# Optimization experiments

Measured on AMD Instinct MI355X. Metric: run time of the kernel, lower is better.

Reference implementation:

```python
import jax, jax.numpy as jnp
import numpy as np

D = 1024
H = 16
HD = D // H  # 64
FF = 4 * D
EPS = 1e-5


def _xavier(key, shape):
    fan_in, fan_out = shape[1], shape[0]
    limit = float(np.sqrt(6.0 / (fan_in + fan_out)))
    return jax.random.uniform(key, shape, jnp.float32, -limit, limit)


def setup_inputs() -> dict:
    key = jax.random.key(0)
    ks = jax.random.split(key, 8)
    x = jax.random.normal(ks[0], (2, 2048, D), jnp.float32)
    return {
        "x": x,
        "w_qkv": _xavier(ks[1], (3 * D, D)),
        "b_qkv": jnp.zeros((3 * D,), jnp.float32),
        "w_out": _xavier(ks[2], (D, D)),
        "b_out": jnp.zeros((D,), jnp.float32),
        "w1": _xavier(ks[3], (FF, D)),
        "b1": jnp.zeros((FF,), jnp.float32),
        "w2": _xavier(ks[4], (D, FF)),
        "b2": jnp.zeros((D,), jnp.float32),
        "ln1_g": jnp.ones((D,), jnp.float32),
        "ln1_b": jnp.zeros((D,), jnp.float32),
        "ln2_g": jnp.ones((D,), jnp.float32),
        "ln2_b": jnp.zeros((D,), jnp.float32),
    }


def _layernorm(x, g, b):
    mu = jnp.mean(x, -1, keepdims=True)
    var = jnp.mean(jnp.square(x - mu), -1, keepdims=True)
    return (x - mu) * jax.lax.rsqrt(var + EPS) * g + b


def reference(x, w_qkv, b_qkv, w_out, b_out, w1, b1, w2, b2,
              ln1_g, ln1_b, ln2_g, ln2_b):
    B, S, _ = x.shape
    # pre-LN attention branch
    h = _layernorm(x, ln1_g, ln1_b)
    qkv = h @ w_qkv.T + b_qkv                      # [B,S,3D]
    qkv = qkv.reshape(B, S, H, 3 * HD).transpose(0, 2, 1, 3)  # [B,H,S,3hd]
    q, k, v = jnp.split(qkv, 3, axis=-1)
    scores = jnp.einsum('bhqd,bhkd->bhqk', q, k) / np.sqrt(HD)
    attn = jax.nn.softmax(scores, axis=-1)
    ctx = jnp.einsum('bhqk,bhkd->bhqd', attn, v)   # [B,H,S,hd]
    ctx = ctx.transpose(0, 2, 1, 3).reshape(B, S, D)
    x = x + (ctx @ w_out.T + b_out)
    # pre-LN MLP branch
    h = _layernorm(x, ln2_g, ln2_b)
    h = jax.nn.relu(h @ w1.T + b1)
    x = x + (h @ w2.T + b2)
    return x
```

## Files before the change

### kernel.cpp

```cpp
#include <hip/hip_runtime.h>
#include <hip/hip_bf16.h>

typedef __attribute__((ext_vector_type(8))) short bf16x8;
typedef __attribute__((ext_vector_type(4))) float f32x4;
typedef __attribute__((ext_vector_type(16))) float f32x16;
typedef __attribute__((ext_vector_type(4))) unsigned short u16x4;
typedef __attribute__((ext_vector_type(4))) unsigned int u32x4;
typedef unsigned short u16;

__device__ __forceinline__ u16 f2bf(float f) {
  unsigned u = __builtin_bit_cast(unsigned, f);
  u += 0x7fffu + ((u >> 16) & 1u);
  return (u16)(u >> 16);
}
__device__ __forceinline__ float bf2f(u16 u) {
  unsigned v = ((unsigned)u) << 16;
  return __builtin_bit_cast(float, v);
}
__device__ __forceinline__ unsigned cvt_pk_bf16(float lo, float hi) {
  unsigned r;
  asm("v_cvt_pk_bf16_f32 %0, %1, %2" : "=v"(r) : "v"(lo), "v"(hi));
  return r;
}
__device__ __forceinline__ float exp2_fast(float x) {
  float r;
  asm("v_exp_f32 %0, %1" : "=v"(r) : "v"(x));
  return r;
}

__device__ __forceinline__ void gl_lds16(const void* g, void* l) {
  __builtin_amdgcn_global_load_lds((const __attribute__((address_space(1))) void*)g,
                                   (__attribute__((address_space(3))) void*)l,
                                   16, 0, 0);
}

__device__ __forceinline__ void bar() {
  asm volatile("" ::: "memory");
  __builtin_amdgcn_s_barrier();
  asm volatile("" ::: "memory");
}

__global__ __launch_bounds__(256) void ln_cvt(const float* __restrict__ x,
                                              const float* __restrict__ g,
                                              const float* __restrict__ b,
                                              u16* __restrict__ out,
                                              const float* __restrict__ wa,
                                              const float* __restrict__ wb,
                                              const float* __restrict__ wc,
                                              const float* __restrict__ wd,
                                              u16* __restrict__ oa,
                                              u16* __restrict__ ob,
                                              u16* __restrict__ oc,
                                              u16* __restrict__ od) {
  __shared__ float red[8];
  const int t = threadIdx.x;
  if (blockIdx.x < 4096) {
    const int row = blockIdx.x;
    const int lane = t & 63, w = t >> 6;
    const float4 v = ((const float4*)(x + (size_t)row * 1024))[t];
    float s = v.x + v.y + v.z + v.w;
    float q = v.x * v.x + v.y * v.y + v.z * v.z + v.w * v.w;
#pragma unroll
    for (int off = 32; off; off >>= 1) {
      s += __shfl_down(s, off);
      q += __shfl_down(q, off);
    }
    if (lane == 0) { red[w] = s; red[4 + w] = q; }
    __syncthreads();
    s = red[0] + red[1] + red[2] + red[3];
    q = red[4] + red[5] + red[6] + red[7];
    const float mu = s * (1.f / 1024.f);
    const float var = q * (1.f / 1024.f) - mu * mu;
    const float rs = rsqrtf(var + 1e-5f);
    const float4 gv = ((const float4*)g)[t];
    const float4 bv = ((const float4*)b)[t];
    u16x4 o;
    o.x = f2bf((v.x - mu) * rs * gv.x + bv.x);
    o.y = f2bf((v.y - mu) * rs * gv.y + bv.y);
    o.z = f2bf((v.z - mu) * rs * gv.z + bv.z);
    o.w = f2bf((v.w - mu) * rs * gv.w + bv.w);
    ((u16x4*)(out + (size_t)row * 1024))[t] = o;
  } else {
    int i = (blockIdx.x - 4096) * 256 + t;
    const int stride = 2048 * 256;
    for (; i < 3145728; i += stride) {
      const float* src;
      u16* dst;
      int j;
      if (i < 786432) { src = wa; dst = oa; j = i; }
      else if (i < 1048576) { src = wb; dst = ob; j = i - 786432; }
      else if (i < 2097152) { src = wc; dst = oc; j = i - 1048576; }
      else { src = wd; dst = od; j = i - 2097152; }
      float4 v = ((const float4*)src)[j];
      u16x4 o;
      o.x = f2bf(v.x); o.y = f2bf(v.y); o.z = f2bf(v.z); o.w = f2bf(v.w);
      ((u16x4*)dst)[j] = o;
    }
  }
}

__global__ __launch_bounds__(256) void ln_k(const float* __restrict__ x,
                                            const float* __restrict__ g,
                                            const float* __restrict__ b,
                                            u16* __restrict__ out) {
  const int row = blockIdx.x;
  const int t = threadIdx.x;
  const int lane = t & 63, w = t >> 6;
  const float4 v = ((const float4*)(x + (size_t)row * 1024))[t];
  float s = v.x + v.y + v.z + v.w;
  float q = v.x * v.x + v.y * v.y + v.z * v.z + v.w * v.w;
#pragma unroll
  for (int off = 32; off; off >>= 1) {
    s += __shfl_down(s, off);
    q += __shfl_down(q, off);
  }
  __shared__ float red[8];
  if (lane == 0) { red[w] = s; red[4 + w] = q; }
  __syncthreads();
  s = red[0] + red[1] + red[2] + red[3];
  q = red[4] + red[5] + red[6] + red[7];
  const float mu = s * (1.f / 1024.f);
  const float var = q * (1.f / 1024.f) - mu * mu;
  const float rs = rsqrtf(var + 1e-5f);
  const float4 gv = ((const float4*)g)[t];
  const float4 bv = ((const float4*)b)[t];
  u16x4 o;
  o.x = f2bf((v.x - mu) * rs * gv.x + bv.x);
  o.y = f2bf((v.y - mu) * rs * gv.y + bv.y);
  o.z = f2bf((v.z - mu) * rs * gv.z + bv.z);
  o.w = f2bf((v.w - mu) * rs * gv.w + bv.w);
  ((u16x4*)(out + (size_t)row * 1024))[t] = o;
}

template <int EPI>
__global__ __launch_bounds__(512, 2) void gemm8(const u16* __restrict__ A,
                                                const u16* __restrict__ B,
                                                const float* __restrict__ bias,
                                                void* __restrict__ outp,
                                                const int N, const int K) {
  __shared__ u16 lds[65536];
  const int t = threadIdx.x;
  const int lane = t & 63, w = t >> 6;
  const int wm = w >> 2, wn = w & 3;
  const int l15 = lane & 15, lhi = lane >> 4;
  const int nbx = gridDim.x;
  const int nwg = nbx * gridDim.y;
  const int orig = blockIdx.y * nbx + blockIdx.x;
  const int cpx = nwg >> 3;
  const int lid = (orig & 7) * cpx + (orig >> 3);
  const long bm = (long)(lid / nbx) * 256, bn = (long)(lid % nbx) * 256;
  const u16* Ab = A + bm * K;
  const u16* Bb = B + bn * K;
  const int nt = K >> 6;
  const int ni2 = nt >> 1;

  const int srow0 = t >> 3, sg0 = (t & 7) ^ (srow0 & 7);
  const int srow1 = 64 + srow0, sg1 = (t & 7) ^ (srow1 & 7);

#define STAGE8(Mb, hf, kt_, dstb)                                             \
  do {                                                                        \
    const long kk_ = (long)(kt_) << 6;                                        \
    gl_lds16(Mb + (size_t)((hf) * 128 + srow0) * K + kk_ + sg0 * 8,           \
             &lds[(dstb) + w * 512]);                                         \
    gl_lds16(Mb + (size_t)((hf) * 128 + srow1) * K + kk_ + sg1 * 8,           \
             &lds[(dstb) + 4096 + w * 512]);                                  \
  } while (0)

#define LOADA(db, mi, fk0, fk1)                                               \
  {                                                                           \
    const int r_ = (mi) * 16 + l15;                                           \
    const int b_ = ((db) * 2 + wm) * 8192 + r_ * 64;                          \
    fk0 = *(const bf16x8*)&lds[b_ + ((lhi ^ (r_ & 7)) << 3)];                 \
    fk1 = *(const bf16x8*)&lds[b_ + (((4 + lhi) ^ (r_ & 7)) << 3)];           \
  }

#define LOADB(db)                                                             \
  _Pragma("unroll")                                                           \
  for (int ni = 0; ni < 4; ++ni) {                                            \
    const int R_ = wn * 64 + ni * 16 + l15;                                   \
    const int b_ = 32768 + ((db) * 2 + (R_ >> 7)) * 8192 + (R_ & 127) * 64;   \
    bq[ni][0] = *(const bf16x8*)&lds[b_ + ((lhi ^ (R_ & 7)) << 3)];           \
    bq[ni][1] = *(const bf16x8*)&lds[b_ + (((4 + lhi) ^ (R_ & 7)) << 3)];     \
  }

#define MM(q, a0k0, a0k1, a1k0, a1k1)                                         \
  __builtin_amdgcn_s_setprio(1);                                              \
  _Pragma("unroll")                                                           \
  for (int ni = 0; ni < 4; ++ni) {                                            \
    acc[2 * (q)][ni] = __builtin_amdgcn_mfma_f32_16x16x32_bf16(               \
        a0k0, bq[ni][0], acc[2 * (q)][ni], 0, 0, 0);                          \
    acc[2 * (q)][ni] = __builtin_amdgcn_mfma_f32_16x16x32_bf16(               \
        a0k1, bq[ni][1], acc[2 * (q)][ni], 0, 0, 0);                          \
    acc[2 * (q) + 1][ni] = __builtin_amdgcn_mfma_f32_16x16x32_bf16(           \
        a1k0, bq[ni][0], acc[2 * (q) + 1][ni], 0, 0, 0);                      \
    acc[2 * (q) + 1][ni] = __builtin_amdgcn_mfma_f32_16x16x32_bf16(           \
        a1k1, bq[ni][1], acc[2 * (q) + 1][ni], 0, 0, 0);                      \
  }                                                                           \
  __builtin_amdgcn_s_setprio(0);

  f32x4 acc[8][4] = {};
  STAGE8(Bb, 0, 0, 32768 + 0);
  STAGE8(Bb, 1, 0, 32768 + 8192);
  STAGE8(Ab, 0, 0, 0);
  STAGE8(Ab, 1, 0, 8192);
  STAGE8(Bb, 0, 1, 32768 + 16384);
  STAGE8(Bb, 1, 1, 32768 + 24576);
  asm volatile("s_waitcnt vmcnt(4)" ::: "memory");
  bar();

  for (int it = 0; it < ni2; ++it) {
    const int t0 = 2 * it, t1 = 2 * it + 1;
    const bool sN = (it + 1) < ni2;
    bf16x8 bq[4][2];
    bf16x8 a0, a1, a2, a3;
    LOADA(0, 0, a0, a1) LOADA(0, 1, a2, a3) LOADB(0);
    STAGE8(Ab, 0, t1, 16384);
    bar();
    MM(0, a0, a1, a2, a3)
    bar();
    LOADA(0, 2, a0, a1) LOADA(0, 3, a2, a3)
    STAGE8(Ab, 1, t1, 24576);
    if (sN) STAGE8(Bb, 0, t0 + 2, 32768 + 0);
    bar();
    MM(1, a0, a1, a2, a3)
    bar();
    LOADA(0, 4, a0, a1) LOADA(0, 5, a2, a3)
    if (sN) STAGE8(Bb, 1, t0 + 2, 32768 + 8192);
    bar();
    MM(2, a0, a1, a2, a3)
    bar();
    LOADA(0, 6, a0, a1) LOADA(0, 7, a2, a3)
    if (sN) asm volatile("s_waitcnt vmcnt(4)" ::: "memory");
    else    asm volatile("s_waitcnt vmcnt(0)" ::: "memory");
    bar();
    MM(3, a0, a1, a2, a3)
    bar();
    LOADA(1, 0, a0, a1) LOADA(1, 1, a2, a3) LOADB(1);
    if (sN) STAGE8(Ab, 0, t0 + 2, 0);
    bar();
    MM(0, a0, a1, a2, a3)
    bar();
    LOADA(1, 2, a0, a1) LOADA(1, 3, a2, a3)
    if (sN) {
      STAGE8(Ab, 1, t0 + 2, 8192);
      STAGE8(Bb, 0, t1 + 2, 32768 + 16384);
    }
    bar();
    MM(1, a0, a1, a2, a3)
    bar();
    LOADA(1, 4, a0, a1) LOADA(1, 5, a2, a3)
    if (sN) STAGE8(Bb, 1, t1 + 2, 32768 + 24576);
    bar();
    MM(2, a0, a1, a2, a3)
    bar();
    LOADA(1, 6, a0, a1) LOADA(1, 7, a2, a3)
    if (sN) asm volatile("s_waitcnt vmcnt(4)" ::: "memory");
    else    asm volatile("s_waitcnt vmcnt(0)" ::: "memory");
    bar();
    MM(3, a0, a1, a2, a3)
    bar();
  }
#undef STAGE8
#undef LOADA
#undef LOADB
#undef MM
  {
    u16* cw = &lds[w * 8192];
#pragma unroll
    for (int ni = 0; ni < 4; ++ni) {
      const long col = bn + wn * 64 + ni * 16 + l15;
      const float bj = bias[col];
      const int cg = ni * 2 + (l15 >> 3);
      const int co = l15 & 7;
#pragma unroll
      for (int mi = 0; mi < 8; ++mi) {
#pragma unroll
        for (int r = 0; r < 4; ++r) {
          float v = acc[mi][ni][r] + bj;
          if constexpr (EPI == 2) v = v > 0.f ? v : 0.f;
          const int row = mi * 16 + lhi * 4 + r;
          cw[row * 64 + (((cg ^ (row & 7)) << 3) | co)] = f2bf(v);
        }
      }
    }
    const long rowbase = bm + wm * 128;
    const long colbase = bn + wn * 64;
#pragma unroll
    for (int p = 0; p < 16; ++p) {
      const int idx = p * 512 + lane * 8;
      const int row = idx >> 6;
      const int cg2 = (idx & 63) >> 3;
      const bf16x8 val = *(const bf16x8*)&cw[row * 64 + ((cg2 ^ (row & 7)) << 3)];
      *(bf16x8*)&((u16*)outp)[(rowbase + row) * N + colbase + cg2 * 8] = val;
    }
  }
}

template <int BM, int BN, int BK, int TH, int WN, int MR, int NR, int EPI>
__global__ __launch_bounds__(TH, 2) void gemm_rot(const u16* __restrict__ A,
                                                  const u16* __restrict__ B,
                                                  const float* __restrict__ bias,
                                                  const float* __restrict__ res,
                                                  void* __restrict__ outp,
                                                  const int N, const int K) {
  constexpr int GPR = BK / 8;
  constexpr int KS = BK / 32;
  constexpr int AELEMS = BM * BK;
  constexpr int BELEMS = BN * BK;
  constexpr int NC = (BM + BN) * GPR / TH;
  static_assert((BM * GPR) % TH == 0 && ((BM + BN) * GPR) % TH == 0, "");
  __shared__ u16 lds[3][AELEMS + BELEMS];
  const int t = threadIdx.x;
  const int lane = t & 63, w = t >> 6;
  const int wm = w / WN, wn = w % WN;
  const int l15 = lane & 15, lhi = lane >> 4;
  const int nbx = gridDim.x;
  const int nwg = nbx * gridDim.y;
  const int orig = blockIdx.y * nbx + blockIdx.x;
  const int cpx = nwg >> 3;
  const int lid = (orig & 7) * cpx + (orig >> 3);
  const long bm = (long)(lid / nbx) * BM, bn = (long)(lid % nbx) * BN;
  const u16* Ab = A + bm * K;
  const u16* Bb = B + bn * K;
  const int nk = K / BK;

#define STAGE(kt_, bufi)                                                      \
  do {                                                                        \
    const long kk_ = (long)(kt_) * BK;                                        \
    _Pragma("unroll")                                                         \
    for (int j = 0; j < NC; ++j) {                                            \
      const int sj = j * TH + t;                                              \
      const u16* src_;                                                        \
      if ((j + 1) * TH <= BM * GPR) {                                         \
        const int row_ = sj / GPR, grp_ = sj % GPR;                           \
        const int g_ = (BK == 32) ? (grp_ ^ ((row_ >> 1) & 3))                \
                                  : (grp_ ^ (row_ & 7));                      \
        src_ = Ab + (size_t)row_ * K + kk_ + g_ * 8;                          \
      } else {                                                                \
        const int sb_ = sj - BM * GPR;                                        \
        const int row_ = sb_ / GPR, grp_ = sb_ % GPR;                         \
        const int g_ = (BK == 32) ? (grp_ ^ ((row_ >> 1) & 3))                \
                                  : (grp_ ^ (row_ & 7));                      \
        src_ = Bb + (size_t)row_ * K + kk_ + g_ * 8;                          \
      }                                                                       \
      gl_lds16(src_, &lds[bufi][(size_t)(j * TH + w * 64) * 8]);              \
    }                                                                         \
  } while (0)

  f32x4 acc[MR][NR] = {};
  STAGE(0, 0);
  STAGE(1, 1);
  for (int i = 0; i < nk; ++i) {
    if (i + 1 < nk) {
      if constexpr (NC == 3)      asm volatile("s_waitcnt vmcnt(3)" ::: "memory");
      else if constexpr (NC == 4) asm volatile("s_waitcnt vmcnt(4)" ::: "memory");
      else                        asm volatile("s_waitcnt vmcnt(6)" ::: "memory");
    } else {
      asm volatile("s_waitcnt vmcnt(0)" ::: "memory");
    }
    bar();
    if (i + 2 < nk) STAGE(i + 2, (i + 2) % 3);
    const u16* bufA = lds[i % 3];
    const u16* bufB = bufA + AELEMS;
    bf16x8 av[MR][KS], bv[NR][KS];
#pragma unroll
    for (int ii = 0; ii < MR; ++ii) {
      const int R = wm * (MR * 16) + ii * 16 + l15;
#pragma unroll
      for (int ks = 0; ks < KS; ++ks) {
        const int pos = (BK == 32) ? (lhi ^ ((R >> 1) & 3))
                                   : ((ks * 4 + lhi) ^ (R & 7));
        av[ii][ks] = *(const bf16x8*)&bufA[R * BK + (pos << 3)];
      }
    }
#pragma unroll
    for (int jj = 0; jj < NR; ++jj) {
      const int R = wn * (NR * 16) + jj * 16 + l15;
#pragma unroll
      for (int ks = 0; ks < KS; ++ks) {
        const int pos = (BK == 32) ? (lhi ^ ((R >> 1) & 3))
                                   : ((ks * 4 + lhi) ^ (R & 7));
        bv[jj][ks] = *(const bf16x8*)&bufB[R * BK + (pos << 3)];
      }
    }
    __builtin_amdgcn_s_setprio(1);
#pragma unroll
    for (int ii = 0; ii < MR; ++ii)
#pragma unroll
      for (int jj = 0; jj < NR; ++jj)
#pragma unroll
        for (int ks = 0; ks < KS; ++ks)
          acc[ii][jj] = __builtin_amdgcn_mfma_f32_16x16x32_bf16(av[ii][ks], bv[jj][ks],
                                                                acc[ii][jj], 0, 0, 0);
    __builtin_amdgcn_s_setprio(0);
  }
#undef STAGE
#pragma unroll
  for (int jj = 0; jj < NR; ++jj) {
    const long col = bn + wn * (NR * 16) + jj * 16 + l15;
    const float bj = bias[col];
#pragma unroll
    for (int ii = 0; ii < MR; ++ii) {
      const long row0 = bm + wm * (MR * 16) + ii * 16 + lhi * 4;
#pragma unroll
      for (int r = 0; r < 4; ++r) {
        const float v = acc[ii][jj][r] + bj;
        const long idx = (row0 + r) * N + col;
        if constexpr (EPI == 0) {
          ((u16*)outp)[idx] = f2bf(v);
        } else if constexpr (EPI == 1) {
          ((float*)outp)[idx] = v + res[idx];
        } else {
          ((u16*)outp)[idx] = f2bf(v > 0.f ? v : 0.f);
        }
      }
    }
  }
}

__global__ __launch_bounds__(256) void vtrans(const u16* __restrict__ qkv,
                                              u16* __restrict__ vt) {
  const int t = threadIdx.x;
  const int bh = blockIdx.y, b = bh >> 4, h = bh & 15;
  const int kvb = blockIdx.x * 64;
  __shared__ u16 tile[64][72];
  const u16* src = qkv + ((size_t)(b * 2048 + kvb)) * 3072 + h * 192 + 128;
#pragma unroll
  for (int rr = 0; rr < 2; ++rr) {
    const int e = rr * 2048 + t * 8;
    const int kv = e >> 6, d = e & 63;
    *(bf16x8*)&tile[kv][d] = *(const bf16x8*)(src + (size_t)kv * 3072 + d);
  }
  __syncthreads();
#pragma unroll
  for (int rr = 0; rr < 2; ++rr) {
    const int e = rr * 2048 + t * 8;
    const int d = e >> 6, kv = e & 63;
    bf16x8 o;
#pragma unroll
    for (int j = 0; j < 8; ++j) o[j] = (short)tile[kv + j][d];
    *(bf16x8*)(vt + ((size_t)bh * 64 + d) * 2048 + kvb + kv) = o;
  }
}

__global__ __launch_bounds__(512, 4) void attn_k(const u16* __restrict__ qkv,
                                                 const u16* __restrict__ vt,
                                                 u16* __restrict__ part0,
                                                 u16* __restrict__ part1,
                                                 float* __restrict__ lbuf) {
  __shared__ u16 smem[16384];
  const int t = threadIdx.x;
  const int lane = t & 63, w = t >> 6;
  const int l31 = lane & 31, hl = lane >> 5;
  const int l7 = l31 & 7;
  const int lid = blockIdx.x + 8 * blockIdx.y + 256 * blockIdx.z;
  const int bh = (lid & 7) * 4 + ((lid >> 3) & 3);
  const int qblk = (lid >> 5) & 7;
  const int sidx = lid >> 8;
  const int b = bh >> 4, h = bh & 15;
  const int qb = qblk * 256 + w * 32;
  const int kvbeg = sidx * 1024;

  const float qscale = 0.125f * 1.44269504f;
  const u16* qp = qkv + ((size_t)(b * 2048 + qb + l31)) * 3072 + h * 192;
  bf16x8 qf[4];
#pragma unroll
  for (int ds = 0; ds < 4; ++ds) {
    bf16x8 v = *(const bf16x8*)(qp + 16 * ds + 8 * hl);
#pragma unroll
    for (int j = 0; j < 8; ++j) v[j] = (short)f2bf(bf2f((u16)v[j]) * qscale);
    qf[ds] = v;
  }

  const int srow = t >> 3, sgc = t & 7;
  const int sswz = (sgc ^ (srow & 7)) * 8;
  const u16* kg0 = qkv + ((size_t)(b * 2048 + srow)) * 3072 + h * 192 + 64 + sswz;
  const u16* vg0 = vt + (size_t)bh * 64 * 2048 + (size_t)srow * 2048 + sswz;

  f32x16 o0 = {}, o1 = {};
  float lsum = 0.f;

#define STAGE(bufi, kv0i)                                              \
  do {                                                                 \
    gl_lds16(kg0 + (size_t)(kv0i) * 3072, &smem[(bufi) * 4096 + w * 512]); \
    gl_lds16(vg0 + (kv0i), &smem[8192 + (bufi) * 4096 + w * 512]);     \
  } while (0)

#define PACK(dst, SA, tl)                                                 \
  do {                                                                    \
    unsigned A0 = cvt_pk_bf16(SA[8 * tl + 0], SA[8 * tl + 1]);            \
    unsigned A1 = cvt_pk_bf16(SA[8 * tl + 2], SA[8 * tl + 3]);            \
    unsigned B0 = cvt_pk_bf16(SA[8 * tl + 4], SA[8 * tl + 5]);            \
    unsigned B1 = cvt_pk_bf16(SA[8 * tl + 6], SA[8 * tl + 7]);            \
    asm volatile("v_permlane32_swap_b32 %0, %1" : "+v"(A0), "+v"(B0));    \
    asm volatile("v_permlane32_swap_b32 %0, %1" : "+v"(A1), "+v"(B1));    \
    u32x4 pv_ = {A0, A1, B0, B1};                                         \
    dst = __builtin_bit_cast(bf16x8, pv_);                                \
  } while (0)

  int buf = 0;
  STAGE(0, kvbeg);
  for (int it = 0; it < 16; ++it) {
    asm volatile("s_waitcnt vmcnt(0)" ::: "memory");
    bar();
    if (it + 1 < 16) STAGE(buf ^ 1, kvbeg + (it + 1) * 64);
    const u16* kbuf = &smem[buf * 4096];
    const u16* vbuf = &smem[8192 + buf * 4096];
    f32x16 sa0 = {}, sa1 = {};
    __builtin_amdgcn_s_setprio(1);
#pragma unroll
    for (int ds = 0; ds < 4; ++ds) {
      const bf16x8 kf0 = *(const bf16x8*)&kbuf[l31 * 64 + (((2 * ds + hl) ^ l7) << 3)];
      const bf16x8 kf1 = *(const bf16x8*)&kbuf[(32 + l31) * 64 + (((2 * ds + hl) ^ l7) << 3)];
      sa0 = __builtin_amdgcn_mfma_f32_32x32x16_bf16(kf0, qf[ds], sa0, 0, 0, 0);
      sa1 = __builtin_amdgcn_mfma_f32_32x32x16_bf16(kf1, qf[ds], sa1, 0, 0, 0);
    }
    __builtin_amdgcn_s_setprio(0);
#pragma unroll
    for (int i = 0; i < 16; ++i) sa0[i] = exp2_fast(sa0[i]);
#pragma unroll
    for (int i = 0; i < 16; ++i) sa1[i] = exp2_fast(sa1[i]);
    const f32x16 ps = sa0 + sa1;
    float s8[8];
#pragma unroll
    for (int i = 0; i < 8; ++i) s8[i] = ps[i] + ps[i + 8];
    const float q0s = (s8[0] + s8[1]) + (s8[2] + s8[3]);
    const float q1s = (s8[4] + s8[5]) + (s8[6] + s8[7]);
    float rsum = q0s + q1s;
    rsum += __shfl_xor(rsum, 32);
    lsum += rsum;
    bf16x8 pf0, pf1, pf2, pf3;
    PACK(pf0, sa0, 0);
    PACK(pf1, sa0, 1);
    PACK(pf2, sa1, 0);
    PACK(pf3, sa1, 1);
    __builtin_amdgcn_s_setprio(1);
#pragma unroll
    for (int t4i = 0; t4i < 4; ++t4i) {
      const bf16x8 vf0 = *(const bf16x8*)&vbuf[l31 * 64 + (((2 * t4i + hl) ^ l7) << 3)];
      const bf16x8 vf1 = *(const bf16x8*)&vbuf[(32 + l31) * 64 + (((2 * t4i + hl) ^ l7) << 3)];
      const bf16x8 pf = (t4i == 0) ? pf0 : (t4i == 1) ? pf1 : (t4i == 2) ? pf2 : pf3;
      o0 = __builtin_amdgcn_mfma_f32_32x32x16_bf16(vf0, pf, o0, 0, 0, 0);
      o1 = __builtin_amdgcn_mfma_f32_32x32x16_bf16(vf1, pf, o1, 0, 0, 0);
    }
    __builtin_amdgcn_s_setprio(0);
    buf ^= 1;
  }
#undef STAGE
#undef PACK
  bar();
  if (lane < 32) {
    lbuf[(size_t)(sidx * 32 + bh) * 2048 + qb + l31] = lsum;
  }
  u16* obase = (sidx == 0) ? part0 : part1;
  u16* ow = &smem[w * 2048];
#pragma unroll
  for (int g2 = 0; g2 < 4; ++g2) {
    uint2 v0, v1;
    v0.x = cvt_pk_bf16(o0[4 * g2 + 0], o0[4 * g2 + 1]);
    v0.y = cvt_pk_bf16(o0[4 * g2 + 2], o0[4 * g2 + 3]);
    v1.x = cvt_pk_bf16(o1[4 * g2 + 0], o1[4 * g2 + 1]);
    v1.y = cvt_pk_bf16(o1[4 * g2 + 2], o1[4 * g2 + 3]);
    *(uint2*)&ow[l31 * 64 + ((g2 ^ l7) << 3) + hl * 4] = v0;
    *(uint2*)&ow[l31 * 64 + (((4 + g2) ^ l7) << 3) + hl * 4] = v1;
  }
#pragma unroll
  for (int p = 0; p < 4; ++p) {
    const int q = 8 * p + (lane >> 3);
    const int gpos = lane & 7;
    const bf16x8 val = *(const bf16x8*)&ow[q * 64 + (gpos << 3)];
    const int gd = gpos ^ (q & 7);
    *(bf16x8*)(obase + ((size_t)(b * 2048 + qb + q)) * 1024 + h * 64 + gd * 8) = val;
  }
}

__global__ __launch_bounds__(256) void attn_merge(const u16* __restrict__ p1,
                                                  const float* __restrict__ lbuf,
                                                  u16* __restrict__ ctx) {
  const int c = blockIdx.x * 256 + threadIdx.x;
  const int row = c >> 7;
  const int b = row >> 11, q = row & 2047;
  const int h = (c >> 3) & 15;
  const int bh = b * 16 + h;
  const float l1 = lbuf[(size_t)bh * 2048 + q];
  const float l2 = lbuf[(size_t)(32 + bh) * 2048 + q];
  const float inv = 1.f / (l1 + l2);
  const bf16x8 v0 = ((const bf16x8*)ctx)[c];
  const bf16x8 v1 = ((const bf16x8*)p1)[c];
  float r[8];
#pragma unroll
  for (int j = 0; j < 8; ++j)
    r[j] = (bf2f((u16)v0[j]) + bf2f((u16)v1[j])) * inv;
  u32x4 ov = {cvt_pk_bf16(r[0], r[1]), cvt_pk_bf16(r[2], r[3]),
              cvt_pk_bf16(r[4], r[5]), cvt_pk_bf16(r[6], r[7])};
  ((u32x4*)ctx)[c] = ov;
}

extern "C" void kernel_launch(void* const* d_in, const int* in_sizes, int n_in,
                              void* d_out, int out_size, void* d_ws, size_t ws_size,
                              hipStream_t stream) {
  const float* x     = (const float*)d_in[0];
  const float* w_qkv = (const float*)d_in[1];
  const float* b_qkv = (const float*)d_in[2];
  const float* w_out = (const float*)d_in[3];
  const float* b_out = (const float*)d_in[4];
  const float* w1    = (const float*)d_in[5];
  const float* b1    = (const float*)d_in[6];
  const float* w2    = (const float*)d_in[7];
  const float* b2    = (const float*)d_in[8];
  const float* ln1g  = (const float*)d_in[9];
  const float* ln1b  = (const float*)d_in[10];
  const float* ln2g  = (const float*)d_in[11];
  const float* ln2b  = (const float*)d_in[12];
  float* out = (float*)d_out;

  u16* wqkv_b = (u16*)d_ws;
  u16* wout_b = wqkv_b + (size_t)3072 * 1024;
  u16* w1_b   = wout_b + (size_t)1024 * 1024;
  u16* w2_b   = w1_b + (size_t)4096 * 1024;
  u16* r1     = w2_b + (size_t)1024 * 4096;
  u16* r2     = r1 + (size_t)4096 * 1024;
  u16* qkvb   = r2;
  u16* vtb    = r2 + (size_t)4096 * 3072;
  float* x2   = (float*)(r2 + (size_t)4096 * 4096);
  u16* part1  = (u16*)x2;
  float* lbuf = (float*)(part1 + (size_t)4096 * 1024);

  ln_cvt<<<6144, 256, 0, stream>>>(x, ln1g, ln1b, r1,
                                   w_qkv, w_out, w1, w2,
                                   wqkv_b, wout_b, w1_b, w2_b);

  gemm8<0><<<dim3(12, 16), 512, 0, stream>>>(r1, wqkv_b, b_qkv, qkvb, 3072, 1024);
  vtrans<<<dim3(32, 32), 256, 0, stream>>>(qkvb, vtb);
  attn_k<<<dim3(8, 32, 2), 512, 0, stream>>>(qkvb, vtb, r1, part1, lbuf);
  attn_merge<<<2048, 256, 0, stream>>>(part1, lbuf, r1);
  gemm_rot<64, 128, 64, 256, 2, 2, 4, 1><<<dim3(8, 64), 256, 0, stream>>>(
      r1, wout_b, b_out, x, x2, 1024, 1024);
  ln_k<<<4096, 256, 0, stream>>>(x2, ln2g, ln2b, r1);
  gemm8<2><<<dim3(16, 16), 512, 0, stream>>>(r1, w1_b, b1, r2, 4096, 1024);
  gemm_rot<64, 128, 64, 256, 2, 2, 4, 1><<<dim3(8, 64), 256, 0, stream>>>(
      r2, w2_b, b2, x2, out, 1024, 4096);
}
```

Baseline: 202.9 us.

## Split attention KV into four partitions and double-buffer rotation GEMM

The attention kernel now splits the KV range into four 512-key chunks instead of two 1024-key chunks. That doubles the grid to 1024 workgroups, and the merge kernel combines four partial outputs and four row sums. Extra partial buffers reuse the output tensor as scratch. Separately, gemm_rot drops from triple to double buffering with a full vmcnt(0) wait, cutting LDS so it can target three workgroups per CU. This trades prefetch depth for occupancy and adds merge traffic in exchange for attention parallelism.

```diff
diff --git a/kernel.cpp b/kernel.cpp
--- a/kernel.cpp
+++ b/kernel.cpp
@@ -297,7 +297,7 @@
 }
 
 template <int BM, int BN, int BK, int TH, int WN, int MR, int NR, int EPI>
-__global__ __launch_bounds__(TH, 2) void gemm_rot(const u16* __restrict__ A,
+__global__ __launch_bounds__(TH, 3) void gemm_rot(const u16* __restrict__ A,
                                                   const u16* __restrict__ B,
                                                   const float* __restrict__ bias,
                                                   const float* __restrict__ res,
@@ -309,7 +309,7 @@
   constexpr int BELEMS = BN * BK;
   constexpr int NC = (BM + BN) * GPR / TH;
   static_assert((BM * GPR) % TH == 0 && ((BM + BN) * GPR) % TH == 0, "");
-  __shared__ u16 lds[3][AELEMS + BELEMS];
+  __shared__ u16 lds[2][AELEMS + BELEMS];
   const int t = threadIdx.x;
   const int lane = t & 63, w = t >> 6;
   const int wm = w / WN, wn = w % WN;
@@ -349,18 +349,11 @@
 
   f32x4 acc[MR][NR] = {};
   STAGE(0, 0);
-  STAGE(1, 1);
   for (int i = 0; i < nk; ++i) {
-    if (i + 1 < nk) {
-      if constexpr (NC == 3)      asm volatile("s_waitcnt vmcnt(3)" ::: "memory");
-      else if constexpr (NC == 4) asm volatile("s_waitcnt vmcnt(4)" ::: "memory");
-      else                        asm volatile("s_waitcnt vmcnt(6)" ::: "memory");
-    } else {
-      asm volatile("s_waitcnt vmcnt(0)" ::: "memory");
-    }
-    bar();
-    if (i + 2 < nk) STAGE(i + 2, (i + 2) % 3);
-    const u16* bufA = lds[i % 3];
+    asm volatile("s_waitcnt vmcnt(0)" ::: "memory");
+    bar();
+    if (i + 1 < nk) STAGE(i + 1, (i + 1) & 1);
+    const u16* bufA = lds[i & 1];
     const u16* bufB = bufA + AELEMS;
     bf16x8 av[MR][KS], bv[NR][KS];
 #pragma unroll
@@ -447,6 +440,8 @@
                                                  const u16* __restrict__ vt,
                                                  u16* __restrict__ part0,
                                                  u16* __restrict__ part1,
+                                                 u16* __restrict__ part2,
+                                                 u16* __restrict__ part3,
                                                  float* __restrict__ lbuf) {
   __shared__ u16 smem[16384];
   const int t = threadIdx.x;
@@ -459,7 +454,7 @@
   const int sidx = lid >> 8;
   const int b = bh >> 4, h = bh & 15;
   const int qb = qblk * 256 + w * 32;
-  const int kvbeg = sidx * 1024;
+  const int kvbeg = sidx * 512;
 
   const float qscale = 0.125f * 1.44269504f;
   const u16* qp = qkv + ((size_t)(b * 2048 + qb + l31)) * 3072 + h * 192;
@@ -500,10 +495,10 @@
 
   int buf = 0;
   STAGE(0, kvbeg);
-  for (int it = 0; it < 16; ++it) {
+  for (int it = 0; it < 8; ++it) {
     asm volatile("s_waitcnt vmcnt(0)" ::: "memory");
     bar();
-    if (it + 1 < 16) STAGE(buf ^ 1, kvbeg + (it + 1) * 64);
+    if (it + 1 < 8) STAGE(buf ^ 1, kvbeg + (it + 1) * 64);
     const u16* kbuf = &smem[buf * 4096];
     const u16* vbuf = &smem[8192 + buf * 4096];
     f32x16 sa0 = {}, sa1 = {};
@@ -552,7 +547,8 @@
   if (lane < 32) {
     lbuf[(size_t)(sidx * 32 + bh) * 2048 + qb + l31] = lsum;
   }
-  u16* obase = (sidx == 0) ? part0 : part1;
+  u16* obase = (sidx == 0) ? part0 : (sidx == 1) ? part1
+              : (sidx == 2) ? part2 : part3;
   u16* ow = &smem[w * 2048];
 #pragma unroll
   for (int g2 = 0; g2 < 4; ++g2) {
@@ -575,6 +571,8 @@
 }
 
 __global__ __launch_bounds__(256) void attn_merge(const u16* __restrict__ p1,
+                                                  const u16* __restrict__ p2,
+                                                  const u16* __restrict__ p3,
                                                   const float* __restrict__ lbuf,
                                                   u16* __restrict__ ctx) {
   const int c = blockIdx.x * 256 + threadIdx.x;
@@ -582,15 +580,19 @@
   const int b = row >> 11, q = row & 2047;
   const int h = (c >> 3) & 15;
   const int bh = b * 16 + h;
-  const float l1 = lbuf[(size_t)bh * 2048 + q];
-  const float l2 = lbuf[(size_t)(32 + bh) * 2048 + q];
-  const float inv = 1.f / (l1 + l2);
+  float lt = 0.f;
+#pragma unroll
+  for (int s = 0; s < 4; ++s) lt += lbuf[(size_t)(s * 32 + bh) * 2048 + q];
+  const float inv = 1.f / lt;
   const bf16x8 v0 = ((const bf16x8*)ctx)[c];
   const bf16x8 v1 = ((const bf16x8*)p1)[c];
+  const bf16x8 v2 = ((const bf16x8*)p2)[c];
+  const bf16x8 v3 = ((const bf16x8*)p3)[c];
   float r[8];
 #pragma unroll
   for (int j = 0; j < 8; ++j)
-    r[j] = (bf2f((u16)v0[j]) + bf2f((u16)v1[j])) * inv;
+    r[j] = ((bf2f((u16)v0[j]) + bf2f((u16)v1[j])) +
+            (bf2f((u16)v2[j]) + bf2f((u16)v3[j]))) * inv;
   u32x4 ov = {cvt_pk_bf16(r[0], r[1]), cvt_pk_bf16(r[2], r[3]),
               cvt_pk_bf16(r[4], r[5]), cvt_pk_bf16(r[6], r[7])};
   ((u32x4*)ctx)[c] = ov;
@@ -625,6 +627,8 @@
   float* x2   = (float*)(r2 + (size_t)4096 * 4096);
   u16* part1  = (u16*)x2;
   float* lbuf = (float*)(part1 + (size_t)4096 * 1024);
+  u16* part2  = (u16*)out;
+  u16* part3  = part2 + (size_t)4096 * 1024;
 
   ln_cvt<<<6144, 256, 0, stream>>>(x, ln1g, ln1b, r1,
                                    w_qkv, w_out, w1, w2,
@@ -632,8 +636,8 @@
 
   gemm8<0><<<dim3(12, 16), 512, 0, stream>>>(r1, wqkv_b, b_qkv, qkvb, 3072, 1024);
   vtrans<<<dim3(32, 32), 256, 0, stream>>>(qkvb, vtb);
-  attn_k<<<dim3(8, 32, 2), 512, 0, stream>>>(qkvb, vtb, r1, part1, lbuf);
-  attn_merge<<<2048, 256, 0, stream>>>(part1, lbuf, r1);
+  attn_k<<<dim3(8, 32, 4), 512, 0, stream>>>(qkvb, vtb, r1, part1, part2, part3, lbuf);
+  attn_merge<<<2048, 256, 0, stream>>>(part1, part2, part3, lbuf, r1);
   gemm_rot<64, 128, 64, 256, 2, 2, 4, 1><<<dim3(8, 64), 256, 0, stream>>>(
       r1, wout_b, b_out, x, x2, 1024, 1024);
   ln_k<<<4096, 256, 0, stream>>>(x2, ln2g, ln2b, r1);
```

Result: slower. 208.4 us (+2.7%).
